# Optimization experiments

Hardware: AMD Instinct MI355X
Metric: run time of the kernel (lower is better)

## Reference

```python
import jax, jax.numpy as jnp
import numpy as np

NUM_NODES = 10000
NUM_EDGES = 160000
IN_CH = 768
TYPE_DIM = 128
HID = 768
OUT = 768
NUM_REL = 3
NUM_NODE_TYPE = 3


def _glorot(key, shape):
    fan_in, fan_out = shape[-2], shape[-1]
    lim = (6.0 / (fan_in + fan_out)) ** 0.5
    return jax.random.uniform(key, shape, jnp.float32, -lim, lim)


def setup_inputs() -> dict:
    key = jax.random.key(0)
    ks = jax.random.split(key, 16)
    d1 = IN_CH + TYPE_DIM  # 896
    inp = {
        "x": jax.random.normal(ks[0], (NUM_NODES, IN_CH), jnp.float32),
        "node_type": jax.random.randint(ks[1], (NUM_NODES,), 0, NUM_NODE_TYPE, jnp.int32),
        "edge_index": jax.random.randint(ks[2], (2, NUM_EDGES), 0, NUM_NODES, jnp.int32),
        "edge_type": jax.random.randint(ks[3], (NUM_EDGES,), 0, NUM_REL, jnp.int32),
        "node_emb": jax.random.normal(ks[4], (NUM_NODE_TYPE, TYPE_DIM), jnp.float32),
        # layer 1: d1 -> d1
        "w_rel1": _glorot(ks[5], (NUM_REL, d1, d1)),
        "w_root1": _glorot(ks[6], (d1, d1)),
        "b1": jnp.zeros((d1,), jnp.float32),
        # layer 2: d1 -> HID
        "w_rel2": _glorot(ks[7], (NUM_REL, d1, HID)),
        "w_root2": _glorot(ks[8], (d1, HID)),
        "b2": jnp.zeros((HID,), jnp.float32),
        # layer 3: HID -> OUT
        "w_rel3": _glorot(ks[9], (NUM_REL, HID, OUT)),
        "w_root3": _glorot(ks[10], (HID, OUT)),
        "b3": jnp.zeros((OUT,), jnp.float32),
    }
    return inp


def rgcn_conv(h, src, dst, edge_type, w_rel, w_root, bias):
    """PyG-style RGCNConv: per-relation linear + per-relation mean aggregation at dst."""
    num_nodes = h.shape[0]
    # per-relation transforms of all nodes: [R, N, out]
    xw = jnp.einsum('nd,rde->rne', h, w_rel)
    # gather the message for each edge according to its relation: [E, out]
    msg = xw[edge_type, src]
    # per-(node, relation) incoming-edge counts for mean aggregation
    onehot = jax.nn.one_hot(edge_type, NUM_REL, dtype=h.dtype)        # [E, R]
    count = jax.ops.segment_sum(onehot, dst, num_segments=num_nodes)  # [N, R]
    inv = jnp.where(count > 0, 1.0 / jnp.maximum(count, 1.0), 0.0)
    msg = msg * inv[dst, edge_type][:, None]
    agg = jax.ops.segment_sum(msg, dst, num_segments=num_nodes)       # [N, out]
    return agg + h @ w_root + bias


def reference(x, node_type, edge_index, edge_type, node_emb,
              w_rel1, w_root1, b1, w_rel2, w_root2, b2, w_rel3, w_root3, b3):
    src, dst = edge_index[0], edge_index[1]
    h = jnp.concatenate([x, node_emb[node_type]], axis=-1)  # [N, 896]
    h = jax.nn.relu(rgcn_conv(h, src, dst, edge_type, w_rel1, w_root1, b1))
    h = jax.nn.relu(rgcn_conv(h, src, dst, edge_type, w_rel2, w_root2, b2))
    h = jax.nn.relu(rgcn_conv(h, src, dst, edge_type, w_rel3, w_root3, b3))
    return h
```

## Files before the change

### kernel.cpp

```cpp
#include <hip/hip_runtime.h>
#include <stdint.h>
#include <stddef.h>

#define N_NODES 10000
#define N_EDGES 160000
#define IN_CH   768
#define TYPE_DIM 128
#define D1      896
#define HID     768
#define N_REL   3
#define NB      (N_NODES * N_REL)

typedef _Float16 f16;
typedef _Float16 f16x4 __attribute__((ext_vector_type(4)));
typedef _Float16 f16x8 __attribute__((ext_vector_type(8)));
typedef float    f32x4 __attribute__((ext_vector_type(4)));

__global__ void zero_ints(int* __restrict__ a, int n) {
    int i = blockIdx.x * 256 + threadIdx.x;
    if (i < n) a[i] = 0;
}

__global__ void concat_f16(const float* __restrict__ x, const int* __restrict__ node_type,
                           const float* __restrict__ node_emb, f16* __restrict__ H) {
    int tid = blockIdx.x * 256 + threadIdx.x;
    int n = tid / (D1 / 4);
    int c = (tid % (D1 / 4)) * 4;
    if (n >= N_NODES) return;
    float4 v;
    if (c < IN_CH) v = *(const float4*)(x + (size_t)n * IN_CH + c);
    else           v = *(const float4*)(node_emb + (size_t)node_type[n] * TYPE_DIM + (c - IN_CH));
    f16x4 o; o[0] = (f16)v.x; o[1] = (f16)v.y; o[2] = (f16)v.z; o[3] = (f16)v.w;
    *(f16x4*)(H + (size_t)n * D1 + c) = o;
}

__global__ void count_kernel(const int* __restrict__ ei, const int* __restrict__ et,
                             int* __restrict__ counts) {
    int e = blockIdx.x * 256 + threadIdx.x;
    if (e >= N_EDGES) return;
    atomicAdd(&counts[ei[N_EDGES + e] * N_REL + et[e]], 1);
}

__global__ void scan_kernel(const int* __restrict__ counts, int* __restrict__ row_ptr) {
    __shared__ int part[1024];
    int t = threadIdx.x;
    const int CH = (NB + 1023) / 1024;
    int s = 0;
    for (int i = 0; i < CH; i++) { int idx = t * CH + i; if (idx < NB) s += counts[idx]; }
    part[t] = s;
    __syncthreads();
    for (int off = 1; off < 1024; off <<= 1) {
        int v = part[t];
        int u = (t >= off) ? part[t - off] : 0;
        __syncthreads();
        part[t] = v + u;
        __syncthreads();
    }
    int base = (t > 0) ? part[t - 1] : 0;
    for (int i = 0; i < CH; i++) {
        int idx = t * CH + i;
        if (idx < NB) { row_ptr[idx] = base; base += counts[idx]; }
    }
    if (t == 1023) row_ptr[NB] = base;
}

__global__ void fill_kernel(const int* __restrict__ ei, const int* __restrict__ et,
                            const int* __restrict__ row_ptr, int* __restrict__ cursor,
                            int* __restrict__ entries) {
    int e = blockIdx.x * 256 + threadIdx.x;
    if (e >= N_EDGES) return;
    int b = ei[N_EDGES + e] * N_REL + et[e];
    int pos = atomicAdd(&cursor[b], 1);
    entries[row_ptr[b] + pos] = ei[e];
}

__global__ void transpose_to_f16(const float* __restrict__ w, int N,
                                 f16* __restrict__ bt, int ldbt, int koff) {
    __shared__ float t[32][33];
    int kb = blockIdx.x * 32, nb = blockIdx.y * 32;
    int tx = threadIdx.x, ty = threadIdx.y;
#pragma unroll
    for (int i = 0; i < 4; i++)
        t[ty * 4 + i][tx] = w[(size_t)(kb + ty * 4 + i) * N + nb + tx];
    __syncthreads();
#pragma unroll
    for (int i = 0; i < 4; i++)
        bt[(size_t)(nb + ty * 4 + i) * ldbt + koff + kb + tx] = (f16)t[tx][ty * 4 + i];
}

template <int DIN>
__global__ __launch_bounds__(256) void aggregate_wave(
    const f16* __restrict__ h, const int* __restrict__ row_ptr,
    const int* __restrict__ entries, f16* __restrict__ out, const int ldout) {
    const int b = blockIdx.x * 4 + (threadIdx.x >> 6);
    const int lane = threadIdx.x & 63;
    constexpr int C2 = DIN / 8 - 64;
    const int beg = row_ptr[b], end = row_ptr[b + 1];
    float a0[8], a1[8];
#pragma unroll
    for (int i = 0; i < 8; i++) { a0[i] = 0.f; a1[i] = 0.f; }
    int e = beg;
    for (; e + 4 <= end; e += 4) {
        const f16* rA = h + (size_t)entries[e] * DIN;
        const f16* rB = h + (size_t)entries[e + 1] * DIN;
        const f16* rC = h + (size_t)entries[e + 2] * DIN;
        const f16* rD = h + (size_t)entries[e + 3] * DIN;
        f16x8 vA0 = *(const f16x8*)(rA + lane * 8);
        f16x8 vB0 = *(const f16x8*)(rB + lane * 8);
        f16x8 vC0 = *(const f16x8*)(rC + lane * 8);
        f16x8 vD0 = *(const f16x8*)(rD + lane * 8);
        if (lane < C2) {
            f16x8 vA1 = *(const f16x8*)(rA + 512 + lane * 8);
            f16x8 vB1 = *(const f16x8*)(rB + 512 + lane * 8);
            f16x8 vC1 = *(const f16x8*)(rC + 512 + lane * 8);
            f16x8 vD1 = *(const f16x8*)(rD + 512 + lane * 8);
#pragma unroll
            for (int i = 0; i < 8; i++)
                a1[i] += ((float)vA1[i] + (float)vB1[i]) + ((float)vC1[i] + (float)vD1[i]);
        }
#pragma unroll
        for (int i = 0; i < 8; i++)
            a0[i] += ((float)vA0[i] + (float)vB0[i]) + ((float)vC0[i] + (float)vD0[i]);
    }
    for (; e + 2 <= end; e += 2) {
        const f16* rA = h + (size_t)entries[e] * DIN;
        const f16* rB = h + (size_t)entries[e + 1] * DIN;
        f16x8 vA0 = *(const f16x8*)(rA + lane * 8);
        f16x8 vB0 = *(const f16x8*)(rB + lane * 8);
        if (lane < C2) {
            f16x8 vA1 = *(const f16x8*)(rA + 512 + lane * 8);
            f16x8 vB1 = *(const f16x8*)(rB + 512 + lane * 8);
#pragma unroll
            for (int i = 0; i < 8; i++) { a1[i] += (float)vA1[i]; a1[i] += (float)vB1[i]; }
        }
#pragma unroll
        for (int i = 0; i < 8; i++) { a0[i] += (float)vA0[i]; a0[i] += (float)vB0[i]; }
    }
    if (e < end) {
        const f16* rA = h + (size_t)entries[e] * DIN;
        f16x8 vA0 = *(const f16x8*)(rA + lane * 8);
        if (lane < C2) {
            f16x8 vA1 = *(const f16x8*)(rA + 512 + lane * 8);
#pragma unroll
            for (int i = 0; i < 8; i++) a1[i] += (float)vA1[i];
        }
#pragma unroll
        for (int i = 0; i < 8; i++) a0[i] += (float)vA0[i];
    }
    const float s = (end > beg) ? 1.0f / (float)(end - beg) : 0.f;
    f16* o = out + (size_t)(b / N_REL) * ldout + (size_t)(b % N_REL) * DIN;
    f16x8 w0, w1;
#pragma unroll
    for (int i = 0; i < 8; i++) { w0[i] = (f16)(a0[i] * s); w1[i] = (f16)(a1[i] * s); }
    *(f16x8*)(o + lane * 8) = w0;
    if (lane < C2) *(f16x8*)(o + 512 + lane * 8) = w1;
}

__device__ __forceinline__ void gload16(const void* g, void* l) {
    __builtin_amdgcn_global_load_lds(
        (const __attribute__((address_space(1))) unsigned int*)g,
        (__attribute__((address_space(3))) unsigned int*)l, 16, 0, 0);
}

__global__ __launch_bounds__(512, 4) void gemm_f16_ilv(
    const f16* __restrict__ A1, const int K1,
    const f16* __restrict__ A2, const int K2,
    const f16* __restrict__ BT, const int ldbt,
    const float* __restrict__ bias,
    const int M, const int N,
    f16* __restrict__ Cf16, const int ldc16, float* __restrict__ Cf32) {
    __shared__ f16 T[2 * 16384];

    const int CB = N >> 7;
    const int nwg = gridDim.x;
    const int q = nwg >> 3, r = nwg & 7;
    const int orig = blockIdx.x;
    const int xcd = orig & 7, pos = orig >> 3;
    const int wg = (xcd < r ? xcd * (q + 1) : r * (q + 1) + (xcd - r) * q) + pos;
    const int x = wg / CB, y = wg - x * CB;
    const int row0 = x * 128, col0 = y * 128;

    const int tid  = threadIdx.x;
    const int lane = tid & 63;
    const int wave = tid >> 6;
    const int wr = wave >> 2, wc = wave & 3;
    const int l16 = lane & 15, hi = lane >> 4;
    const int key = l16 & 7;
    const int pAf = (hi ^ key) * 8;
    const int pBf = ((4 | hi) ^ key) * 8;

    f32x4 acc[4][2];
#pragma unroll
    for (int m = 0; m < 4; m++)
#pragma unroll
        for (int n = 0; n < 2; n++) acc[m][n] = (f32x4){0.f, 0.f, 0.f, 0.f};

    const int r_  = tid >> 3;
    const int sl  = (tid & 7) ^ (r_ & 7);
    const bool isA = sl < 4;
    const int colA = sl * 8;
    const int colB = (sl - 4) * 8;
    const f16* pLo[2]; const f16* pHi[2];
#pragma unroll
    for (int j = 0; j < 2; j++) {
        const int rr = r_ + 64 * j;
        if (isA) {
            pLo[j] = A1 + (size_t)(row0 + rr) * K1 + colA;
            pHi[j] = A2 + (size_t)(row0 + rr) * K2 + colA - K1;
        } else {
            pLo[j] = BT + (size_t)(col0 + rr) * ldbt + colB;
            pHi[j] = pLo[j];
        }
    }

    const int KT = K1 + K2;
    const int nt = KT >> 6;

#define STAGE(t) do {                                                  \
        const int k0_ = (t) * 64;                                      \
        f16* l_ = T + ((t) & 1) * 16384 + tid * 8;                     \
        _Pragma("unroll")                                              \
        for (int j = 0; j < 2; j++) {                                  \
            const f16* s_ = ((k0_ < K1) ? pLo[j] : pHi[j]) + k0_;      \
            gload16(s_,      l_ + j * 4096);                           \
            gload16(s_ + 32, l_ + 8192 + j * 4096);                    \
        }                                                              \
    } while (0)

    STAGE(0);
    for (int t = 0; t < nt; ++t) {
        if (t + 1 < nt) {
            STAGE(t + 1);
            asm volatile("s_waitcnt vmcnt(4)" ::: "memory");
        } else {
            asm volatile("s_waitcnt vmcnt(0)" ::: "memory");
        }
        __builtin_amdgcn_s_barrier();

        const f16* Tb = T + (t & 1) * 16384;
        f16x8 af[2][4], bf[2][2];
#pragma unroll
        for (int h = 0; h < 2; h++) {
#pragma unroll
            for (int m = 0; m < 4; m++)
                af[h][m] = *(const f16x8*)(Tb + h * 8192 + (wr * 64 + m * 16 + l16) * 64 + pAf);
#pragma unroll
            for (int n = 0; n < 2; n++)
                bf[h][n] = *(const f16x8*)(Tb + h * 8192 + (wc * 32 + n * 16 + l16) * 64 + pBf);
        }
#pragma unroll
        for (int h = 0; h < 2; h++)
#pragma unroll
            for (int m = 0; m < 4; m++)
#pragma unroll
                for (int n = 0; n < 2; n++)
                    acc[m][n] = __builtin_amdgcn_mfma_f32_16x16x32_f16(af[h][m], bf[h][n], acc[m][n], 0, 0, 0);

        asm volatile("s_barrier" ::: "memory");
    }
#undef STAGE

    const int hi4 = hi * 4;
#pragma unroll
    for (int m = 0; m < 4; m++) {
#pragma unroll
        for (int n = 0; n < 2; n++) {
            const int col = col0 + wc * 32 + n * 16 + l16;
            const float bv = bias[col];
#pragma unroll
            for (int rr2 = 0; rr2 < 4; rr2++) {
                const int row = row0 + wr * 64 + m * 16 + hi4 + rr2;
                if (row < M) {
                    float v = acc[m][n][rr2] + bv;
                    v = v > 0.f ? v : 0.f;
                    if (Cf16) Cf16[(size_t)row * ldc16 + col] = (f16)v;
                    else      Cf32[(size_t)row * N + col] = v;
                }
            }
        }
    }
}

extern "C" void kernel_launch(void* const* d_in, const int* in_sizes, int n_in,
                              void* d_out, int out_size, void* d_ws, size_t ws_size,
                              hipStream_t stream) {
    const float* x         = (const float*)d_in[0];
    const int*   node_type = (const int*)d_in[1];
    const int*   ei        = (const int*)d_in[2];
    const int*   et        = (const int*)d_in[3];
    const float* node_emb  = (const float*)d_in[4];
    const float* w_rel1    = (const float*)d_in[5];
    const float* w_root1   = (const float*)d_in[6];
    const float* b1        = (const float*)d_in[7];
    const float* w_rel2    = (const float*)d_in[8];
    const float* w_root2   = (const float*)d_in[9];
    const float* b2        = (const float*)d_in[10];
    const float* w_rel3    = (const float*)d_in[11];
    const float* w_root3   = (const float*)d_in[12];
    const float* b3        = (const float*)d_in[13];

    char* ws = (char*)d_ws;
    f16* AGG = (f16*)(ws + 0);
    f16* Ha  = (f16*)(ws + 53760000);
    f16* Hb  = (f16*)(ws + 71680000);
    f16* BT1 = (f16*)(ws + 89600000);
    f16* BT2 = (f16*)(ws + 96022528);
    f16* BT3 = (f16*)(ws + 101527552);
    int* counts  = (int*)(ws + 106246144);
    int* cursor  = (int*)(ws + 106366144);
    int* row_ptr = (int*)(ws + 106486144);
    int* entries = (int*)(ws + 106606148);

    zero_ints<<<(2 * NB + 255) / 256, 256, 0, stream>>>(counts, 2 * NB);
    concat_f16<<<(N_NODES * (D1 / 4)) / 256 + 1, 256, 0, stream>>>(x, node_type, node_emb, Ha);
    count_kernel<<<N_EDGES / 256, 256, 0, stream>>>(ei, et, counts);
    scan_kernel<<<1, 1024, 0, stream>>>(counts, row_ptr);
    fill_kernel<<<N_EDGES / 256, 256, 0, stream>>>(ei, et, row_ptr, cursor, entries);

    {
        dim3 b(32, 8);
        transpose_to_f16<<<dim3(2688 / 32, 896 / 32), b, 0, stream>>>(w_rel1, 896, BT1, 3584, 0);
        transpose_to_f16<<<dim3(896 / 32, 896 / 32), b, 0, stream>>>(w_root1, 896, BT1, 3584, 2688);
        transpose_to_f16<<<dim3(2688 / 32, 768 / 32), b, 0, stream>>>(w_rel2, 768, BT2, 3584, 0);
        transpose_to_f16<<<dim3(896 / 32, 768 / 32), b, 0, stream>>>(w_root2, 768, BT2, 3584, 2688);
        transpose_to_f16<<<dim3(2304 / 32, 768 / 32), b, 0, stream>>>(w_rel3, 768, BT3, 3072, 0);
        transpose_to_f16<<<dim3(768 / 32, 768 / 32), b, 0, stream>>>(w_root3, 768, BT3, 3072, 2304);
    }

    const int RB = (N_NODES + 127) / 128;

    aggregate_wave<D1><<<NB / 4, 256, 0, stream>>>(Ha, row_ptr, entries, AGG, 2688);
    gemm_f16_ilv<<<RB * 7, 512, 0, stream>>>(AGG, 2688, Ha, 896, BT1, 3584, b1,
                                             N_NODES, 896, Hb, 896, nullptr);
    aggregate_wave<D1><<<NB / 4, 256, 0, stream>>>(Hb, row_ptr, entries, AGG, 2688);
    gemm_f16_ilv<<<RB * 6, 512, 0, stream>>>(AGG, 2688, Hb, 896, BT2, 3584, b2,
                                             N_NODES, 768, Ha, 768, nullptr);
    aggregate_wave<HID><<<NB / 4, 256, 0, stream>>>(Ha, row_ptr, entries, AGG, 2304);
    gemm_f16_ilv<<<RB * 6, 512, 0, stream>>>(AGG, 2304, Ha, 768, BT3, 3072, b3,
                                             N_NODES, 768, nullptr, 0, (float*)d_out);
}
```

Before: 427.2 us.

## Split K halves across wave groups with 64x64 warp tiles and LDS reduction

Each 128x128 tile is still computed by 8 waves, but waves are now split into two groups that each handle one half of every 64-wide K slice. Each wave owns a 64x64 output subtile instead of 64x32. This halves the LDS fragment reads per MFMA, since each wave loads 4 A and 4 B fragments for 16 MFMAs rather than 8 A and 4 B for 16. The cost is double the accumulator registers, which may hurt occupancy at launch_bounds(512,4), plus an extra LDS reduction pass and syncs in the epilogue.

```diff
diff --git a/kernel.cpp b/kernel.cpp
--- a/kernel.cpp
+++ b/kernel.cpp
@@ -173,27 +173,30 @@
 
     const int CB = N >> 7;
     const int nwg = gridDim.x;
-    const int q = nwg >> 3, r = nwg & 7;
+    const int q8 = nwg >> 3, r8 = nwg & 7;
     const int orig = blockIdx.x;
     const int xcd = orig & 7, pos = orig >> 3;
-    const int wg = (xcd < r ? xcd * (q + 1) : r * (q + 1) + (xcd - r) * q) + pos;
+    const int wg = (xcd < r8 ? xcd * (q8 + 1) : r8 * (q8 + 1) + (xcd - r8) * q8) + pos;
     const int x = wg / CB, y = wg - x * CB;
     const int row0 = x * 128, col0 = y * 128;
 
     const int tid  = threadIdx.x;
     const int lane = tid & 63;
     const int wave = tid >> 6;
-    const int wr = wave >> 2, wc = wave & 3;
+    const int h    = wave >> 2;
+    const int q    = wave & 3;
+    const int wr = q >> 1, wc = q & 1;
     const int l16 = lane & 15, hi = lane >> 4;
+    const int hi4 = hi * 4;
     const int key = l16 & 7;
     const int pAf = (hi ^ key) * 8;
     const int pBf = ((4 | hi) ^ key) * 8;
 
-    f32x4 acc[4][2];
+    f32x4 acc[4][4];
 #pragma unroll
     for (int m = 0; m < 4; m++)
 #pragma unroll
-        for (int n = 0; n < 2; n++) acc[m][n] = (f32x4){0.f, 0.f, 0.f, 0.f};
+        for (int n = 0; n < 4; n++) acc[m][n] = (f32x4){0.f, 0.f, 0.f, 0.f};
 
     const int r_  = tid >> 3;
     const int sl  = (tid & 7) ^ (r_ & 7);
@@ -237,41 +240,54 @@
         }
         __builtin_amdgcn_s_barrier();
 
-        const f16* Tb = T + (t & 1) * 16384;
-        f16x8 af[2][4], bf[2][2];
-#pragma unroll
-        for (int h = 0; h < 2; h++) {
-#pragma unroll
-            for (int m = 0; m < 4; m++)
-                af[h][m] = *(const f16x8*)(Tb + h * 8192 + (wr * 64 + m * 16 + l16) * 64 + pAf);
-#pragma unroll
-            for (int n = 0; n < 2; n++)
-                bf[h][n] = *(const f16x8*)(Tb + h * 8192 + (wc * 32 + n * 16 + l16) * 64 + pBf);
-        }
-#pragma unroll
-        for (int h = 0; h < 2; h++)
-#pragma unroll
-            for (int m = 0; m < 4; m++)
-#pragma unroll
-                for (int n = 0; n < 2; n++)
-                    acc[m][n] = __builtin_amdgcn_mfma_f32_16x16x32_f16(af[h][m], bf[h][n], acc[m][n], 0, 0, 0);
+        const f16* Tb = T + (t & 1) * 16384 + h * 8192;
+        f16x8 af[4], bf[4];
+#pragma unroll
+        for (int m = 0; m < 4; m++)
+            af[m] = *(const f16x8*)(Tb + (wr * 64 + m * 16 + l16) * 64 + pAf);
+#pragma unroll
+        for (int n = 0; n < 4; n++)
+            bf[n] = *(const f16x8*)(Tb + (wc * 64 + n * 16 + l16) * 64 + pBf);
+#pragma unroll
+        for (int m = 0; m < 4; m++)
+#pragma unroll
+            for (int n = 0; n < 4; n++)
+                acc[m][n] = __builtin_amdgcn_mfma_f32_16x16x32_f16(af[m], bf[n], acc[m][n], 0, 0, 0);
 
         asm volatile("s_barrier" ::: "memory");
     }
 #undef STAGE
 
-    const int hi4 = hi * 4;
+    __syncthreads();
+    float* Rf = (float*)T;
+    if (h == 1) {
+#pragma unroll
+        for (int m = 0; m < 4; m++)
+#pragma unroll
+            for (int n = 0; n < 4; n++)
+#pragma unroll
+                for (int j = 0; j < 4; j++) {
+                    const int lr = m * 16 + hi4 + j;
+                    const int lc = (n * 16 + l16) ^ (((lr >> 2) & 1) << 4);
+                    Rf[q * 4096 + lr * 64 + lc] = acc[m][n][j];
+                }
+    }
+    __syncthreads();
+    if (h == 1) return;
+
 #pragma unroll
     for (int m = 0; m < 4; m++) {
 #pragma unroll
-        for (int n = 0; n < 2; n++) {
-            const int col = col0 + wc * 32 + n * 16 + l16;
+        for (int n = 0; n < 4; n++) {
+            const int col = col0 + wc * 64 + n * 16 + l16;
             const float bv = bias[col];
 #pragma unroll
-            for (int rr2 = 0; rr2 < 4; rr2++) {
-                const int row = row0 + wr * 64 + m * 16 + hi4 + rr2;
+            for (int j = 0; j < 4; j++) {
+                const int lr = m * 16 + hi4 + j;
+                const int lc = (n * 16 + l16) ^ (((lr >> 2) & 1) << 4);
+                const int row = row0 + wr * 64 + lr;
                 if (row < M) {
-                    float v = acc[m][n][rr2] + bv;
+                    float v = acc[m][n][j] + Rf[q * 4096 + lr * 64 + lc] + bv;
                     v = v > 0.f ? v : 0.f;
                     if (Cf16) Cf16[(size_t)row * ldc16 + col] = (f16)v;
                     else      Cf32[(size_t)row * N + col] = v;
```

Measured after the change: 429.5 us. No clear change (+0.5%).
